# Kernel optimization log

Hardware: AMD Instinct MI355X
Metric: run time of the kernel (lower is better)

Reference implementation:

```python
import jax, jax.numpy as jnp
import numpy as np

B, S, D_IN, D_OUT = 4, 2048, 1024, 1024


def setup_inputs() -> dict:
    key = jax.random.key(0)
    k1, k2, k3, k4 = jax.random.split(key, 4)
    scale = 1.0 / np.sqrt(D_IN)
    return {
        "x": jax.random.normal(k1, (B, S, D_IN), dtype=jnp.float32),
        "W_q": jax.random.normal(k2, (D_OUT, D_IN), dtype=jnp.float32) * scale,
        "W_k": jax.random.normal(k3, (D_OUT, D_IN), dtype=jnp.float32) * scale,
        "W_v": jax.random.normal(k4, (D_OUT, D_IN), dtype=jnp.float32) * scale,
    }


def reference(x, W_q, W_k, W_v):
    # torch nn.Linear: y = x @ W.T (bias=False)
    q = jnp.einsum("bsd,od->bso", x, W_q)
    k = jnp.einsum("bsd,od->bso", x, W_k)
    v = jnp.einsum("bsd,od->bso", x, W_v)
    s = q.shape[1]
    scores = jnp.einsum("bqo,bko->bqk", q, k)  # [B, S, S]
    causal = jnp.triu(jnp.ones((s, s), dtype=bool), k=1)
    scores = jnp.where(causal, -jnp.inf, scores)
    inv_sqrt_d = 1.0 / jnp.sqrt(jnp.asarray(q.shape[-1], scores.dtype))
    attn = jax.nn.softmax(scores * inv_sqrt_d, axis=-1)
    # dropout p=0.0 -> identity (deterministic reference)
    return jnp.einsum("bqk,bko->bqo", attn, v)
```

## Files before the change

### kernel.cpp

```cpp
#include <hip/hip_runtime.h>

typedef unsigned short u16;
typedef unsigned int u32;
typedef __bf16 bf16x8 __attribute__((ext_vector_type(8)));
typedef float f32x4 __attribute__((ext_vector_type(4)));

#define AS1 __attribute__((address_space(1)))
#define AS3 __attribute__((address_space(3)))

__device__ inline u16 f2bf(float f) {
  union { float f; unsigned u; } a; a.f = f;
  unsigned u = a.u;
  return (u16)((u + 0x7fffu + ((u >> 16) & 1u)) >> 16);
}
__device__ inline float bf2f(u16 h) {
  union { unsigned u; float f; } a; a.u = ((u32)h) << 16; return a.f;
}

__global__ __launch_bounds__(256) void cvt_all_kernel(
    const float* __restrict__ x, const float* __restrict__ wq,
    const float* __restrict__ wk, const float* __restrict__ wv,
    u16* __restrict__ xb, u16* __restrict__ wqb,
    u16* __restrict__ wkb, u16* __restrict__ wvb) {
  int bid = blockIdx.x;
  const float* in; u16* out;
  if (bid < 8192) { in = x; out = xb; }
  else if (bid < 9216) { in = wq; out = wqb; bid -= 8192; }
  else if (bid < 10240) { in = wk; out = wkb; bid -= 9216; }
  else { in = wv; out = wvb; bid -= 10240; }
  size_t i = ((size_t)bid * 256 + threadIdx.x) * 4;
  float4 v = *(const float4*)(in + i);
  ushort4 o;
  o.x = f2bf(v.x); o.y = f2bf(v.y); o.z = f2bf(v.z); o.w = f2bf(v.w);
  *(ushort4*)(out + i) = o;
}

template <typename CT, int BN>
__device__ __forceinline__ void gemm_core(
    u16* __restrict__ lds,
    const u16* __restrict__ A, const u16* __restrict__ B, CT* __restrict__ C,
    int nt, int lda, int ldb, int ldc, int m0, int n0) {
  constexpr int ABUF = 16384;
  constexpr int BBUF = BN * 64;
  constexpr int BSW = BN / 64;
  constexpr int NI = BN / 64;

  const int tid = threadIdx.x;
  const int ln = tid & 63, wv = tid >> 6;
  const int wr = wv >> 2, wc = wv & 3;

  auto sweep = [&](const u16* src, int ld, int t, int s, int base) {
    const int c = s * 512 + tid;
    const int row = c >> 3, slot = c & 7;
    const int col = (slot ^ (row & 7)) * 8;
    __builtin_amdgcn_global_load_lds(
        (const AS1 void*)(src + (size_t)row * ld + (size_t)t * 64 + col),
        (AS3 void*)(&lds[base + c * 8]), 16, 0, 0);
  };

  f32x4 acc[8][NI] = {};

#pragma unroll
  for (int s = 0; s < BSW; ++s) sweep(B, ldb, 0, s, 2 * ABUF);
#pragma unroll
  for (int s = 0; s < 4; ++s) sweep(A, lda, 0, s, 0);
  if (nt > 1) {
#pragma unroll
    for (int s = 0; s < BSW; ++s) sweep(B, ldb, 1, s, 2 * ABUF + BBUF);
#pragma unroll
    for (int s = 0; s < 4; ++s) sweep(A, lda, 1, s, ABUF);
    if constexpr (BSW == 4) asm volatile("s_waitcnt vmcnt(8)" ::: "memory");
    else                    asm volatile("s_waitcnt vmcnt(6)" ::: "memory");
  } else {
    asm volatile("s_waitcnt vmcnt(0)" ::: "memory");
  }
  __builtin_amdgcn_s_barrier();

  for (int t = 0; t < nt; ++t) {
    const int p = t & 1;
    const u16* La = &lds[p * ABUF];
    const u16* Lb = &lds[2 * ABUF + p * BBUF];
    bf16x8 bfr[NI][2];
#pragma unroll
    for (int q = 0; q < 4; ++q) {
      if (q == 0) {
        __builtin_amdgcn_sched_barrier(0);
#pragma unroll
        for (int ni = 0; ni < NI; ++ni)
#pragma unroll
          for (int ks = 0; ks < 2; ++ks) {
            const int row = wc * (BN / 4) + ni * 16 + (ln & 15);
            const int kc = ks * 4 + (ln >> 4);
            bfr[ni][ks] = *(const bf16x8*)&Lb[row * 64 + ((kc ^ (row & 7)) << 3)];
          }
      }
      bf16x8 afr[2][2];
#pragma unroll
      for (int mi = 0; mi < 2; ++mi)
#pragma unroll
        for (int ks = 0; ks < 2; ++ks) {
          const int row = wr * 128 + (q * 2 + mi) * 16 + (ln & 15);
          const int kc = ks * 4 + (ln >> 4);
          afr[mi][ks] = *(const bf16x8*)&La[row * 64 + ((kc ^ (row & 7)) << 3)];
        }
      if (q == 0)      { if (t >= 1 && t + 1 < nt) { sweep(A, lda, t + 1, 0, (p ^ 1) * ABUF); sweep(A, lda, t + 1, 1, (p ^ 1) * ABUF); } }
      else if (q == 1) { if (t >= 1 && t + 1 < nt) { sweep(A, lda, t + 1, 2, (p ^ 1) * ABUF); sweep(A, lda, t + 1, 3, (p ^ 1) * ABUF); } }
      else if (q == 2) { if (t + 2 < nt) { sweep(B, ldb, t + 2, 0, 2 * ABUF + p * BBUF); if (BSW == 4) sweep(B, ldb, t + 2, 1, 2 * ABUF + p * BBUF); } }
      else             { if (t + 2 < nt) { if (BSW == 4) { sweep(B, ldb, t + 2, 2, 2 * ABUF + p * BBUF); sweep(B, ldb, t + 2, 3, 2 * ABUF + p * BBUF); } else { sweep(B, ldb, t + 2, 1, 2 * ABUF + p * BBUF); } } }

      __builtin_amdgcn_s_barrier();
      __builtin_amdgcn_s_setprio(1);
#pragma unroll
      for (int mi = 0; mi < 2; ++mi)
#pragma unroll
        for (int ni = 0; ni < NI; ++ni)
#pragma unroll
          for (int ks = 0; ks < 2; ++ks)
            acc[q * 2 + mi][ni] = __builtin_amdgcn_mfma_f32_16x16x32_bf16(
                afr[mi][ks], bfr[ni][ks], acc[q * 2 + mi][ni], 0, 0, 0);
      __builtin_amdgcn_s_setprio(0);
      if (q == 3) {
        if (t + 2 < nt) {
          if constexpr (BSW == 4) asm volatile("s_waitcnt vmcnt(4)" ::: "memory");
          else                    asm volatile("s_waitcnt vmcnt(2)" ::: "memory");
        } else if (t + 1 < nt) {
          asm volatile("s_waitcnt vmcnt(0)" ::: "memory");
        }
      }
      __builtin_amdgcn_s_barrier();
    }
  }

#pragma unroll
  for (int mi = 0; mi < 8; ++mi) {
    const int rbase = m0 + wr * 128 + mi * 16 + (ln >> 4) * 4;
#pragma unroll
    for (int ni = 0; ni < NI; ++ni) {
      const int col = n0 + wc * (BN / 4) + ni * 16 + (ln & 15);
#pragma unroll
      for (int r = 0; r < 4; ++r) {
        const float v = acc[mi][ni][r];
        CT* ptr = &C[(size_t)(rbase + r) * ldc + col];
        if constexpr (sizeof(CT) == 4) *(float*)ptr = v;
        else                           *ptr = f2bf(v);
      }
    }
  }
}

__global__ __launch_bounds__(512, 2) void proj_qk_kernel(
    const u16* __restrict__ xb, const u16* __restrict__ wqb,
    const u16* __restrict__ wkb, u16* __restrict__ Qb, u16* __restrict__ Kb) {
  __shared__ __align__(16) u16 lds[65536];
  const int bid = blockIdx.x;
  const int w = bid >> 7, r = bid & 127;
  const int rb = r >> 2, n0 = (r & 3) * 256;
  const u16* B = w ? wkb : wqb;
  u16* C = w ? Kb : Qb;
  gemm_core<u16, 256>(lds, xb + (size_t)rb * 256 * 1024, B + (size_t)n0 * 1024,
                      C, 16, 1024, 1024, 1024, rb * 256, n0);
}

__global__ __launch_bounds__(512, 2) void qktvt_kernel(
    const u16* __restrict__ Qb, const u16* __restrict__ Kb, u16* __restrict__ Sb16,
    const u16* __restrict__ wvb, const u16* __restrict__ xb, u16* __restrict__ VTb) {
  __shared__ __align__(16) u16 lds[65536];
  const int bid = blockIdx.x;
  const int item = (bid & 7) * 32 + (bid >> 3);
  if (item < 144) {
    const int z = item / 36, xt = item % 36;
    int m = 0;
    while ((m + 1) * (m + 2) / 2 <= xt) ++m;
    const int n = xt - m * (m + 1) / 2;
    gemm_core<u16, 256>(lds,
        Qb + ((size_t)z * 2048 + m * 256) * 1024,
        Kb + ((size_t)z * 2048 + n * 256) * 1024,
        Sb16 + (size_t)z * 2048 * 2048,
        16, 1024, 1024, 2048, m * 256, n * 256);
  } else {
    const int j = item - 144;
    const int z = j / 28, r2 = j % 28, d = r2 / 7, kb = r2 % 7;
    gemm_core<u16, 256>(lds, wvb + (size_t)d * 256 * 1024,
                        xb + (size_t)z * 2048 * 1024 + (size_t)kb * 256 * 1024,
                        VTb + (size_t)z * 1024 * 2048,
                        16, 1024, 1024, 2048, d * 256, kb * 256);
  }
}

__global__ __launch_bounds__(512, 2) void smvt_kernel(
    u16* __restrict__ Sb16, float* __restrict__ R,
    const u16* __restrict__ wvb, const u16* __restrict__ xb) {
  __shared__ __align__(16) u16 lds[65536];
  const int bid = blockIdx.x;
  const int tid = threadIdx.x;
  if (bid < 32) {
    const int z = bid >> 3, r = bid & 7;
    const int d = r >> 1, h = r & 1;
    const u16* A = wvb + (size_t)d * 256 * 1024 + h * 512;
    const u16* B = xb + ((size_t)z * 2048 + 1792) * 1024 + h * 512;
    float* C = R + (size_t)z * 2097152 + 1572864 + (d * 2 + h) * 65536;
    gemm_core<float, 256>(lds, A, B, C, 8, 1024, 1024, 256, 0, 0);
    return;
  }
  const int j = bid - 32;
  const int m = 7 - (j >> 6), z = (j >> 4) & 3, s = j & 15;
  const int iters = (m + 2) >> 1;
  const int wvid = tid >> 6, lane = tid & 63;
  u16* S0 = Sb16 + (size_t)z * 2048 * 2048;
  for (int rr = wvid; rr < 16; rr += 8) {
    const int r = m * 256 + s * 16 + rr;
    u16* row = S0 + (size_t)r * 2048;
    float vals[4][8];
    float mx = -3.4e38f;
#pragma unroll
    for (int it2 = 0; it2 < 4; ++it2)
      if (it2 < iters) {
        const int idx8 = it2 * 512 + lane * 8;
        uint4 w = *(const uint4*)(row + idx8);
        const u32 ws[4] = {w.x, w.y, w.z, w.w};
#pragma unroll
        for (int e = 0; e < 8; ++e) {
          const u16 hb = (u16)(ws[e >> 1] >> ((e & 1) * 16));
          const float xv = bf2f(hb) * 0.03125f;
          vals[it2][e] = (idx8 + e <= r) ? xv : -3.4e38f;
          mx = fmaxf(mx, vals[it2][e]);
        }
      }
#pragma unroll
    for (int o = 32; o; o >>= 1) mx = fmaxf(mx, __shfl_xor(mx, o, 64));
    float sum = 0.f;
#pragma unroll
    for (int it2 = 0; it2 < 4; ++it2)
      if (it2 < iters) {
#pragma unroll
        for (int e = 0; e < 8; ++e) {
          const float pp = __expf(vals[it2][e] - mx);
          vals[it2][e] = pp;
          sum += pp;
        }
      }
#pragma unroll
    for (int o = 32; o; o >>= 1) sum += __shfl_xor(sum, o, 64);
    const float rcp = 1.f / sum;
#pragma unroll
    for (int it2 = 0; it2 < 4; ++it2)
      if (it2 < iters) {
        const int idx8 = it2 * 512 + lane * 8;
        uint4 w;
        u32 wo[4];
#pragma unroll
        for (int e2 = 0; e2 < 4; ++e2) {
          const u16 lo = f2bf(vals[it2][e2 * 2] * rcp);
          const u16 hi = f2bf(vals[it2][e2 * 2 + 1] * rcp);
          wo[e2] = (u32)lo | ((u32)hi << 16);
        }
        w.x = wo[0]; w.y = wo[1]; w.z = wo[2]; w.w = wo[3];
        *(uint4*)(row + idx8) = w;
      }
  }
}

__global__ __launch_bounds__(256) void vtfix_kernel(const float* __restrict__ R,
                                                    u16* __restrict__ VTb) {
  const int bid = blockIdx.x;
  const int z = bid >> 3, q = bid & 7;
  const int d = q >> 1, rh = q & 1;
  const float* P0 = R + (size_t)z * 2097152 + 1572864 + (d * 2 + 0) * 65536;
  const float* P1 = R + (size_t)z * 2097152 + 1572864 + (d * 2 + 1) * 65536;
  for (int k = threadIdx.x; k < 128 * 64; k += 256) {
    const int dp = rh * 128 + (k >> 6), c4 = (k & 63) * 4;
    float4 a = *(const float4*)(P0 + (size_t)dp * 256 + c4);
    float4 b = *(const float4*)(P1 + (size_t)dp * 256 + c4);
    ushort4 o;
    o.x = f2bf(a.x + b.x); o.y = f2bf(a.y + b.y);
    o.z = f2bf(a.z + b.z); o.w = f2bf(a.w + b.w);
    *(ushort4*)(VTb + (size_t)z * 1024 * 2048 + (size_t)(d * 256 + dp) * 2048 +
                1792 + c4) = o;
  }
}

__constant__ signed char CPM[16] = {5,5,7,7,7,6,4,4,6,6,3,3,1,2,2,0};
__constant__ signed char CPK[16] = {0,12,0,11,22,0,0,10,10,19,0,8,0,0,6,0};
__constant__ signed char CPN[16] = {12,12,11,11,10,10,10,10,9,9,8,8,8,6,6,4};
__constant__ signed char CPS[16] = {0,1,0,1,2,0,0,1,1,2,0,1,0,0,1,0};

__global__ __launch_bounds__(512, 2) void pv_kernel(
    const u16* __restrict__ P, const u16* __restrict__ VTb,
    float* __restrict__ out, float* __restrict__ R) {
  __shared__ __align__(16) u16 lds[65536];
  const int cls = blockIdx.x, n = blockIdx.y;
  const size_t z = blockIdx.z;
  const int m = CPM[cls], k0 = CPK[cls], ntc = CPN[cls], sl = CPS[cls];
  const u16* Ap = P + z * 2048 * 2048 + (size_t)m * 256 * 2048 + (size_t)k0 * 64;
  const u16* Bp = VTb + z * 1024 * 2048 + (size_t)n * 256 * 2048 + (size_t)k0 * 64;
  float* Cp;
  if (sl == 0)      Cp = out + z * 2048 * 1024;
  else if (sl == 1) Cp = R + z * 2097152 - (size_t)512 * 1024;
  else              Cp = R + z * 2097152;
  gemm_core<float, 256>(lds, Ap, Bp, Cp, ntc, 2048, 2048, 1024, m * 256, n * 256);
}

__global__ __launch_bounds__(256) void reduce_kernel(float* __restrict__ out,
                                                     const float* __restrict__ R) {
  const int j = blockIdx.x;
  const int m = 2 + (j >> 5), z = (j >> 3) & 3, s = j & 7;
  float* ob = out + (size_t)z * 2048 * 1024;
  const float* s1 = R + (size_t)z * 2097152;
  const float* s2 = s1 + 1572864;
  const int r0 = m * 256 + s * 32;
  for (int k = threadIdx.x; k < 32 * 256; k += 256) {
    const int rr = r0 + (k >> 8), cc = k & 255;
    float4 o = ((float4*)(ob + (size_t)rr * 1024))[cc];
    float4 a = ((const float4*)(s1 + (size_t)(rr - 512) * 1024))[cc];
    o.x += a.x; o.y += a.y; o.z += a.z; o.w += a.w;
    if (m >= 6) {
      float4 b = ((const float4*)(s2 + (size_t)(rr - 1536) * 1024))[cc];
      o.x += b.x; o.y += b.y; o.z += b.z; o.w += b.w;
    }
    ((float4*)(ob + (size_t)rr * 1024))[cc] = o;
  }
}

extern "C" void kernel_launch(void* const* d_in, const int* in_sizes, int n_in,
                              void* d_out, int out_size, void* d_ws, size_t ws_size,
                              hipStream_t stream) {
  const float* x  = (const float*)d_in[0];
  const float* Wq = (const float*)d_in[1];
  const float* Wk = (const float*)d_in[2];
  const float* Wv = (const float*)d_in[3];
  float* out = (float*)d_out;

  char* ws = (char*)d_ws;
  u16* xb   = (u16*)(ws);
  u16* wqb  = (u16*)(ws + (16ul << 20));
  u16* wkb  = (u16*)(ws + (18ul << 20));
  u16* wvb  = (u16*)(ws + (20ul << 20));
  u16* Qb   = (u16*)(ws + (22ul << 20));
  u16* Kb   = (u16*)(ws + (38ul << 20));
  u16* VTb  = (u16*)(ws + (54ul << 20));
  u16* Sb16 = (u16*)(ws + (70ul << 20));
  float* R  = (float*)(ws + (102ul << 20));

  cvt_all_kernel<<<11264, 256, 0, stream>>>(x, Wq, Wk, Wv, xb, wqb, wkb, wvb);

  proj_qk_kernel<<<256, 512, 0, stream>>>(xb, wqb, wkb, Qb, Kb);

  qktvt_kernel<<<256, 512, 0, stream>>>(Qb, Kb, Sb16, wvb, xb, VTb);

  smvt_kernel<<<544, 512, 0, stream>>>(Sb16, R, wvb, xb);

  vtfix_kernel<<<32, 256, 0, stream>>>(R, VTb);

  pv_kernel<<<dim3(16, 4, 4), 512, 0, stream>>>(Sb16, VTb, out, R);

  reduce_kernel<<<192, 256, 0, stream>>>(out, R);
}
```

Baseline: 161.0 us.

## Split tail V projection four ways and store split-K partials as bf16

The leftover V-projection tile computed inside smvt_kernel is now split four ways along K instead of two, giving 64 smaller blocks that overlap with the softmax work, and vtfix sums four partial buffers. The pv_kernel split-K partial outputs are now written as bf16 instead of fp32 and read back and widened in reduce_kernel. This halves the bytes written and read for the partial sums, in exchange for rounding the partial accumulations to bf16, which lowers output precision. The workspace layout of R is reorganized to fit the new fp32 and bf16 regions.

```diff
diff --git a/kernel.cpp b/kernel.cpp
--- a/kernel.cpp
+++ b/kernel.cpp
@@ -193,16 +193,16 @@
   __shared__ __align__(16) u16 lds[65536];
   const int bid = blockIdx.x;
   const int tid = threadIdx.x;
-  if (bid < 32) {
-    const int z = bid >> 3, r = bid & 7;
-    const int d = r >> 1, h = r & 1;
-    const u16* A = wvb + (size_t)d * 256 * 1024 + h * 512;
-    const u16* B = xb + ((size_t)z * 2048 + 1792) * 1024 + h * 512;
-    float* C = R + (size_t)z * 2097152 + 1572864 + (d * 2 + h) * 65536;
-    gemm_core<float, 256>(lds, A, B, C, 8, 1024, 1024, 256, 0, 0);
+  if (bid < 64) {
+    const int z = bid >> 4, r = bid & 15;
+    const int d = r >> 2, h = r & 3;
+    const u16* A = wvb + (size_t)d * 256 * 1024 + h * 256;
+    const u16* B = xb + ((size_t)z * 2048 + 1792) * 1024 + h * 256;
+    float* C = R + (size_t)z * 2097152 + (d * 4 + h) * 65536;
+    gemm_core<float, 256>(lds, A, B, C, 4, 1024, 1024, 256, 0, 0);
     return;
   }
-  const int j = bid - 32;
+  const int j = bid - 64;
   const int m = 7 - (j >> 6), z = (j >> 4) & 3, s = j & 15;
   const int iters = (m + 2) >> 1;
   const int wvid = tid >> 6, lane = tid & 63;
@@ -265,15 +265,20 @@
   const int bid = blockIdx.x;
   const int z = bid >> 3, q = bid & 7;
   const int d = q >> 1, rh = q & 1;
-  const float* P0 = R + (size_t)z * 2097152 + 1572864 + (d * 2 + 0) * 65536;
-  const float* P1 = R + (size_t)z * 2097152 + 1572864 + (d * 2 + 1) * 65536;
+  const float* P0 = R + (size_t)z * 2097152 + (d * 4 + 0) * 65536;
+  const float* P1 = P0 + 65536;
+  const float* P2 = P0 + 131072;
+  const float* P3 = P0 + 196608;
   for (int k = threadIdx.x; k < 128 * 64; k += 256) {
     const int dp = rh * 128 + (k >> 6), c4 = (k & 63) * 4;
-    float4 a = *(const float4*)(P0 + (size_t)dp * 256 + c4);
-    float4 b = *(const float4*)(P1 + (size_t)dp * 256 + c4);
+    const size_t off = (size_t)dp * 256 + c4;
+    float4 a = *(const float4*)(P0 + off);
+    float4 b = *(const float4*)(P1 + off);
+    float4 c = *(const float4*)(P2 + off);
+    float4 e = *(const float4*)(P3 + off);
     ushort4 o;
-    o.x = f2bf(a.x + b.x); o.y = f2bf(a.y + b.y);
-    o.z = f2bf(a.z + b.z); o.w = f2bf(a.w + b.w);
+    o.x = f2bf(a.x + b.x + c.x + e.x); o.y = f2bf(a.y + b.y + c.y + e.y);
+    o.z = f2bf(a.z + b.z + c.z + e.z); o.w = f2bf(a.w + b.w + c.w + e.w);
     *(ushort4*)(VTb + (size_t)z * 1024 * 2048 + (size_t)(d * 256 + dp) * 2048 +
                 1792 + c4) = o;
   }
@@ -286,36 +291,41 @@
 
 __global__ __launch_bounds__(512, 2) void pv_kernel(
     const u16* __restrict__ P, const u16* __restrict__ VTb,
-    float* __restrict__ out, float* __restrict__ R) {
+    float* __restrict__ out, char* __restrict__ R) {
   __shared__ __align__(16) u16 lds[65536];
   const int cls = blockIdx.x, n = blockIdx.y;
   const size_t z = blockIdx.z;
   const int m = CPM[cls], k0 = CPK[cls], ntc = CPN[cls], sl = CPS[cls];
   const u16* Ap = P + z * 2048 * 2048 + (size_t)m * 256 * 2048 + (size_t)k0 * 64;
   const u16* Bp = VTb + z * 1024 * 2048 + (size_t)n * 256 * 2048 + (size_t)k0 * 64;
-  float* Cp;
-  if (sl == 0)      Cp = out + z * 2048 * 1024;
-  else if (sl == 1) Cp = R + z * 2097152 - (size_t)512 * 1024;
-  else              Cp = R + z * 2097152;
-  gemm_core<float, 256>(lds, Ap, Bp, Cp, ntc, 2048, 2048, 1024, m * 256, n * 256);
+  if (sl == 0) {
+    gemm_core<float, 256>(lds, Ap, Bp, out + z * 2048 * 1024, ntc,
+                          2048, 2048, 1024, m * 256, n * 256);
+  } else if (sl == 1) {
+    u16* s1 = (u16*)(R + z * (8ul << 20) + (4ul << 20)) - (size_t)512 * 1024;
+    gemm_core<u16, 256>(lds, Ap, Bp, s1, ntc, 2048, 2048, 1024, m * 256, n * 256);
+  } else {
+    u16* s2 = (u16*)(R + z * (8ul << 20) + (7ul << 20)) - (size_t)1536 * 1024;
+    gemm_core<u16, 256>(lds, Ap, Bp, s2, ntc, 2048, 2048, 1024, m * 256, n * 256);
+  }
 }
 
 __global__ __launch_bounds__(256) void reduce_kernel(float* __restrict__ out,
-                                                     const float* __restrict__ R) {
+                                                     const char* __restrict__ R) {
   const int j = blockIdx.x;
   const int m = 2 + (j >> 5), z = (j >> 3) & 3, s = j & 7;
   float* ob = out + (size_t)z * 2048 * 1024;
-  const float* s1 = R + (size_t)z * 2097152;
-  const float* s2 = s1 + 1572864;
+  const u16* s1 = (const u16*)(R + (size_t)z * (8ul << 20) + (4ul << 20));
+  const u16* s2 = (const u16*)(R + (size_t)z * (8ul << 20) + (7ul << 20));
   const int r0 = m * 256 + s * 32;
   for (int k = threadIdx.x; k < 32 * 256; k += 256) {
     const int rr = r0 + (k >> 8), cc = k & 255;
     float4 o = ((float4*)(ob + (size_t)rr * 1024))[cc];
-    float4 a = ((const float4*)(s1 + (size_t)(rr - 512) * 1024))[cc];
-    o.x += a.x; o.y += a.y; o.z += a.z; o.w += a.w;
+    ushort4 a = ((const ushort4*)(s1 + (size_t)(rr - 512) * 1024))[cc];
+    o.x += bf2f(a.x); o.y += bf2f(a.y); o.z += bf2f(a.z); o.w += bf2f(a.w);
     if (m >= 6) {
-      float4 b = ((const float4*)(s2 + (size_t)(rr - 1536) * 1024))[cc];
-      o.x += b.x; o.y += b.y; o.z += b.z; o.w += b.w;
+      ushort4 b = ((const ushort4*)(s2 + (size_t)(rr - 1536) * 1024))[cc];
+      o.x += bf2f(b.x); o.y += bf2f(b.y); o.z += bf2f(b.z); o.w += bf2f(b.w);
     }
     ((float4*)(ob + (size_t)rr * 1024))[cc] = o;
   }
@@ -339,7 +349,7 @@
   u16* Kb   = (u16*)(ws + (38ul << 20));
   u16* VTb  = (u16*)(ws + (54ul << 20));
   u16* Sb16 = (u16*)(ws + (70ul << 20));
-  float* R  = (float*)(ws + (102ul << 20));
+  char* R   = ws + (102ul << 20);
 
   cvt_all_kernel<<<11264, 256, 0, stream>>>(x, Wq, Wk, Wv, xb, wqb, wkb, wvb);
 
@@ -347,9 +357,9 @@
 
   qktvt_kernel<<<256, 512, 0, stream>>>(Qb, Kb, Sb16, wvb, xb, VTb);
 
-  smvt_kernel<<<544, 512, 0, stream>>>(Sb16, R, wvb, xb);
-
-  vtfix_kernel<<<32, 256, 0, stream>>>(R, VTb);
+  smvt_kernel<<<576, 512, 0, stream>>>(Sb16, (float*)R, wvb, xb);
+
+  vtfix_kernel<<<32, 256, 0, stream>>>((const float*)R, VTb);
 
   pv_kernel<<<dim3(16, 4, 4), 512, 0, stream>>>(Sb16, VTb, out, R);
 
```

Result: no change. 161.0 us (-0.0%).
